# Performance work log

Measured on AMD Instinct MI355X. Metric: run time of the kernel, lower is better.

## Reference

```python
import jax, jax.numpy as jnp
import numpy as np
from jax import lax

NUM_SPLIT = 16
DCT = 7
# top16 frequency indices (first 16 of the top lists)
MAPPER_X = np.array([0, 0, 6, 0, 0, 1, 1, 4, 5, 1, 3, 0, 0, 0, 3, 2], dtype=np.int32)
MAPPER_Y = np.array([0, 1, 0, 5, 2, 0, 2, 0, 0, 6, 0, 4, 6, 3, 5, 2], dtype=np.int32)


def _dct_table():
    pos = np.arange(DCT)
    freq = np.arange(DCT)[:, None]
    d = np.cos(np.pi * freq * (pos + 0.5) / DCT) / np.sqrt(DCT)
    d[1:] *= np.sqrt(2.0)
    return d.astype(np.float32)  # (7, 7): [freq, pos]


def _gconv(x, w, b, groups):
    y = lax.conv_general_dilated(x, w, (2, 2), 'VALID',
                                 dimension_numbers=('NCHW', 'OIHW', 'NCHW'),
                                 feature_group_count=groups)
    return y + b[None, :, None, None]


def setup_inputs() -> dict:
    key = jax.random.key(0)
    ks = jax.random.split(key, 7)
    n, c, h, w = 32, 512, 56, 56
    r = 16
    return {
        'x': jax.random.normal(ks[0], (n, c, h, w), jnp.float32),
        'conv1_w': jax.random.normal(ks[1], (NUM_SPLIT, c // NUM_SPLIT, 3, 3), jnp.float32) * 0.05,
        'conv1_b': jax.random.normal(ks[2], (NUM_SPLIT,), jnp.float32) * 0.05,
        'conv2_w': jax.random.normal(ks[3], (NUM_SPLIT, 1, 3, 3), jnp.float32) * 0.3,
        'conv2_b': jax.random.normal(ks[4], (NUM_SPLIT,), jnp.float32) * 0.3,
        'w1': jax.random.normal(ks[5], (c // r, c), jnp.float32) * 0.05,
        'w2': jax.random.normal(ks[6], (c, c // r), jnp.float32) * 0.2,
    }


def reference(x, conv1_w, conv1_b, conv2_w, conv2_b, w1, w2):
    n, c, h, w = x.shape
    c_part = c // NUM_SPLIT
    D = jnp.asarray(_dct_table(), x.dtype)
    mx = jnp.asarray(MAPPER_X)
    my = jnp.asarray(MAPPER_Y)

    # adaptive_avg_pool2d to 7x7 (h,w divisible by 7 -> exact block mean)
    xp = x.reshape(n, c, DCT, h // DCT, DCT, w // DCT).mean(axis=(3, 5))

    # filters_predicted: grouped conv 7x7 -> 3x3 -> 1x1
    a1 = jax.nn.hard_sigmoid(_gconv(xp, conv1_w, conv1_b, NUM_SPLIT))
    v = _gconv(a1, conv2_w, conv2_b, NUM_SPLIT).reshape(n, NUM_SPLIT)
    # adaptive_avg_pool1d(1 -> 16) repeats v; matmul with ones(16,1) sums -> v * 16
    pred = jnp.clip(v * NUM_SPLIT, 0.0, NUM_SPLIT - 1.1)

    left = pred.astype(jnp.int32)   # (n, 16)
    frac = pred - left
    right = left + 1

    def dct_weights(idx):  # idx (n,16) -> per-split 7x7 DCT filters (n,16,7,7)
        fx = D[mx[idx]]  # (n,16,7)
        fy = D[my[idx]]
        return fx[..., :, None] * fy[..., None, :]

    xp_s = xp.reshape(n, NUM_SPLIT, c_part, DCT, DCT)
    res_l = jnp.einsum('nskhw,nshw->nsk', xp_s, dct_weights(left)) * (1.0 - frac)[:, :, None]
    res_r = jnp.einsum('nskhw,nshw->nsk', xp_s, dct_weights(right)) * frac[:, :, None]
    s = (res_l + res_r).reshape(n, c)

    hmid = jax.nn.hard_sigmoid(s @ w1.T)
    cw = jax.nn.sigmoid(hmid @ w2.T)  # (n, c)
    return x * cw[:, :, None, None]
```

## Files before the change

kernel.cpp:

```cpp
#include <hip/hip_runtime.h>

#define N_   32
#define C_   512
#define H_   56
#define W_   56
#define S_   16
#define CP_  32
#define HW_  (H_*W_)
#define TOT_ ((size_t)N_*C_*HW_)

typedef float f32x4 __attribute__((ext_vector_type(4)));

__constant__ int d_mx[16] = {0,0,6,0,0,1,1,4,5,1,3,0,0,0,3,2};
__constant__ int d_my[16] = {0,1,0,5,2,0,2,0,0,6,0,4,6,3,5,2};

__global__ void __launch_bounds__(256) pool_kernel(const float* __restrict__ x,
                                                   float* __restrict__ xp) {
    __shared__ float part[784];
    int plane = blockIdx.x;
    int t = threadIdx.x;
    const f32x4* src = reinterpret_cast<const f32x4*>(x + (size_t)plane * HW_);
    f32x4 u0 = src[t];
    f32x4 u1 = src[t + 256];
    f32x4 u2 = src[t + 512];
    f32x4 u3;
    if (t < 16) u3 = src[t + 768];
    part[t]       = u0.x + u0.y + u0.z + u0.w;
    part[t + 256] = u1.x + u1.y + u1.z + u1.w;
    part[t + 512] = u2.x + u2.y + u2.z + u2.w;
    if (t < 16) part[t + 768] = u3.x + u3.y + u3.z + u3.w;
    __syncthreads();
    if (t < 49) {
        int rb = t / 7, cb = t - rb * 7;
        const float* p = &part[rb * 8 * 14 + cb * 2];
        float s = 0.f;
#pragma unroll
        for (int r = 0; r < 8; ++r) s += p[r * 14] + p[r * 14 + 1];
        xp[(size_t)plane * 49 + t] = s * (1.0f / 64.0f);
    }
}

__global__ void __launch_bounds__(256) head_kernel(
        const float* __restrict__ xp,
        const float* __restrict__ c1w, const float* __restrict__ c1b,
        const float* __restrict__ c2w, const float* __restrict__ c2b,
        const float* __restrict__ w1,  const float* __restrict__ w2,
        float* __restrict__ cwout) {
    __shared__ float sD[49];
    __shared__ float a1[S_ * 9];
    __shared__ float wcomb[S_ * 49];
    __shared__ float svec[C_];
    __shared__ float hpart[256];
    __shared__ float hmid[32];
    __shared__ float sfrac[S_];
    __shared__ int   sleft[S_];

    const int n = blockIdx.x, t = threadIdx.x;
    const float* xpn = xp + (size_t)n * C_ * 49;

    if (t >= 192 && t < 241) {
        int u = t - 192, f = u / 7, p = u - f * 7;
        float v = cosf(3.14159265358979323846f * f * (p + 0.5f) / 7.0f) * 0.3779644730092272f;
        if (f >= 1) v *= 1.4142135623730951f;
        sD[u] = v;
    }
    if (t < S_ * 9) {
        int s = t / 9, o = t - s * 9, oi = o / 3, oj = o - oi * 3;
        float acc = c1b[s];
        const float* xb = xpn + s * CP_ * 49;
        const float* wb = c1w + s * CP_ * 9;
        for (int ic = 0; ic < CP_; ++ic) {
#pragma unroll
            for (int ki = 0; ki < 3; ++ki)
#pragma unroll
                for (int kj = 0; kj < 3; ++kj)
                    acc += xb[ic * 49 + (oi * 2 + ki) * 7 + (oj * 2 + kj)]
                         * wb[ic * 9 + ki * 3 + kj];
        }
        a1[t] = fminf(fmaxf(acc + 3.f, 0.f), 6.f) * (1.f / 6.f);
    }
    __syncthreads();

    if (t < S_) {
        float acc = c2b[t];
#pragma unroll
        for (int k = 0; k < 9; ++k) acc += a1[t * 9 + k] * c2w[t * 9 + k];
        float pred = fminf(fmaxf(acc * 16.f, 0.f), 14.9f);
        int l = (int)pred;
        sleft[t] = l;
        sfrac[t] = pred - (float)l;
    }
    __syncthreads();

    for (int i = t; i < S_ * 49; i += 256) {
        int s = i / 49, p = i - s * 49, hh = p / 7, ww = p - hh * 7;
        int l = sleft[s], r = l + 1;
        float fr = sfrac[s];
        wcomb[i] = (1.f - fr) * sD[d_mx[l] * 7 + hh] * sD[d_my[l] * 7 + ww]
                 +        fr  * sD[d_mx[r] * 7 + hh] * sD[d_my[r] * 7 + ww];
    }
    __syncthreads();

#pragma unroll
    for (int q = 0; q < 2; ++q) {
        int ch = t + q * 256;
        const float* xb = xpn + ch * 49;
        const float* wb = &wcomb[(ch >> 5) * 49];
        float acc = 0.f;
#pragma unroll
        for (int p = 0; p < 49; ++p) acc += xb[p] * wb[p];
        svec[ch] = acc;
    }
    __syncthreads();

    {
        int o = t >> 3, g = t & 7;
        const f32x4* wv = reinterpret_cast<const f32x4*>(w1 + o * C_ + g * 64);
        const f32x4* sv = reinterpret_cast<const f32x4*>(&svec[g * 64]);
        float acc = 0.f;
#pragma unroll
        for (int j = 0; j < 16; ++j) {
            f32x4 a = sv[j], b = wv[j];
            acc += a.x * b.x + a.y * b.y + a.z * b.z + a.w * b.w;
        }
        hpart[t] = acc;
    }
    __syncthreads();
    if (t < 32) {
        float acc = 0.f;
#pragma unroll
        for (int g = 0; g < 8; ++g) acc += hpart[t * 8 + g];
        hmid[t] = fminf(fmaxf(acc + 3.f, 0.f), 6.f) * (1.f / 6.f);
    }
    __syncthreads();

#pragma unroll
    for (int q = 0; q < 2; ++q) {
        int ch = t + q * 256;
        const f32x4* wr = reinterpret_cast<const f32x4*>(w2 + ch * 32);
        const f32x4* hv = reinterpret_cast<const f32x4*>(hmid);
        float acc = 0.f;
#pragma unroll
        for (int j = 0; j < 8; ++j) {
            f32x4 h = hv[j], b = wr[j];
            acc += h.x * b.x + h.y * b.y + h.z * b.z + h.w * b.w;
        }
        cwout[n * C_ + ch] = 1.f / (1.f + expf(-acc));
    }
}

__global__ void __launch_bounds__(256) scale_kernel(const float* __restrict__ x,
                                                    const float* __restrict__ cw,
                                                    float* __restrict__ out) {
    int plane = blockIdx.x;
    int t = threadIdx.x;
    float wsc = cw[plane];
    const f32x4* src = reinterpret_cast<const f32x4*>(x + (size_t)plane * HW_);
    f32x4* dst = reinterpret_cast<f32x4*>(out + (size_t)plane * HW_);

    f32x4 u0 = src[t];
    f32x4 u1 = src[t + 256];
    f32x4 u2 = src[t + 512];
    f32x4 u3;
    if (t < 16) u3 = src[t + 768];

    u0 *= wsc;
    u1 *= wsc;
    u2 *= wsc;

    __builtin_nontemporal_store(u0, dst + t);
    __builtin_nontemporal_store(u1, dst + t + 256);
    __builtin_nontemporal_store(u2, dst + t + 512);
    if (t < 16) {
        u3 *= wsc;
        __builtin_nontemporal_store(u3, dst + t + 768);
    }
}

extern "C" void kernel_launch(void* const* d_in, const int* in_sizes, int n_in,
                              void* d_out, int out_size, void* d_ws, size_t ws_size,
                              hipStream_t stream) {
    const float* x   = (const float*)d_in[0];
    const float* c1w = (const float*)d_in[1];
    const float* c1b = (const float*)d_in[2];
    const float* c2w = (const float*)d_in[3];
    const float* c2b = (const float*)d_in[4];
    const float* w1  = (const float*)d_in[5];
    const float* w2  = (const float*)d_in[6];
    float* out = (float*)d_out;

    float* xp    = (float*)d_ws;
    float* cwbuf = xp + (size_t)N_ * C_ * 49;

    pool_kernel<<<N_ * C_, 256, 0, stream>>>(x, xp);
    head_kernel<<<N_, 256, 0, stream>>>(xp, c1w, c1b, c2w, c2b, w1, w2, cwbuf);
    scale_kernel<<<N_ * C_, 256, 0, stream>>>(x, cwbuf, out);
}
```

Before: 393.2 us.

## Fuse pooling and head into one kernel using last-block atomic counter

The pooling and head kernels are merged into one kernel. Each block pools one plane, then bumps a per-sample atomic counter, and the last block to finish for a sample runs the head computation. This removes a kernel launch and the serial head kernel that ran only 32 blocks, so head work for each sample can overlap with pooling of other samples. In exchange it adds a memset launch, threadfences and atomics, and the fused kernel uses more shared memory, which may lower occupancy during the bandwidth-bound pooling phase.

After: 1.064 ms. 2.71x slower.

```diff
diff --git a/kernel.cpp b/kernel.cpp
--- a/kernel.cpp
+++ b/kernel.cpp
@@ -14,38 +14,16 @@
 __constant__ int d_mx[16] = {0,0,6,0,0,1,1,4,5,1,3,0,0,0,3,2};
 __constant__ int d_my[16] = {0,1,0,5,2,0,2,0,0,6,0,4,6,3,5,2};
 
-__global__ void __launch_bounds__(256) pool_kernel(const float* __restrict__ x,
-                                                   float* __restrict__ xp) {
-    __shared__ float part[784];
-    int plane = blockIdx.x;
-    int t = threadIdx.x;
-    const f32x4* src = reinterpret_cast<const f32x4*>(x + (size_t)plane * HW_);
-    f32x4 u0 = src[t];
-    f32x4 u1 = src[t + 256];
-    f32x4 u2 = src[t + 512];
-    f32x4 u3;
-    if (t < 16) u3 = src[t + 768];
-    part[t]       = u0.x + u0.y + u0.z + u0.w;
-    part[t + 256] = u1.x + u1.y + u1.z + u1.w;
-    part[t + 512] = u2.x + u2.y + u2.z + u2.w;
-    if (t < 16) part[t + 768] = u3.x + u3.y + u3.z + u3.w;
-    __syncthreads();
-    if (t < 49) {
-        int rb = t / 7, cb = t - rb * 7;
-        const float* p = &part[rb * 8 * 14 + cb * 2];
-        float s = 0.f;
-#pragma unroll
-        for (int r = 0; r < 8; ++r) s += p[r * 14] + p[r * 14 + 1];
-        xp[(size_t)plane * 49 + t] = s * (1.0f / 64.0f);
-    }
-}
-
-__global__ void __launch_bounds__(256) head_kernel(
-        const float* __restrict__ xp,
+__global__ void __launch_bounds__(256) pool_head_kernel(
+        const float* __restrict__ x,
+        float* __restrict__ xp,
+        int* __restrict__ counters,
         const float* __restrict__ c1w, const float* __restrict__ c1b,
         const float* __restrict__ c2w, const float* __restrict__ c2b,
         const float* __restrict__ w1,  const float* __restrict__ w2,
         float* __restrict__ cwout) {
+    __shared__ float part[784];
+    __shared__ int   lastflag;
     __shared__ float sD[49];
     __shared__ float a1[S_ * 9];
     __shared__ float wcomb[S_ * 49];
@@ -55,7 +33,42 @@
     __shared__ float sfrac[S_];
     __shared__ int   sleft[S_];
 
-    const int n = blockIdx.x, t = threadIdx.x;
+    const int plane = blockIdx.x;
+    const int t = threadIdx.x;
+
+    {
+        const f32x4* src = reinterpret_cast<const f32x4*>(x + (size_t)plane * HW_);
+        f32x4 u0 = src[t];
+        f32x4 u1 = src[t + 256];
+        f32x4 u2 = src[t + 512];
+        f32x4 u3;
+        if (t < 16) u3 = src[t + 768];
+        part[t]       = u0.x + u0.y + u0.z + u0.w;
+        part[t + 256] = u1.x + u1.y + u1.z + u1.w;
+        part[t + 512] = u2.x + u2.y + u2.z + u2.w;
+        if (t < 16) part[t + 768] = u3.x + u3.y + u3.z + u3.w;
+        __syncthreads();
+        if (t < 49) {
+            int rb = t / 7, cb = t - rb * 7;
+            const float* p = &part[rb * 8 * 14 + cb * 2];
+            float s = 0.f;
+#pragma unroll
+            for (int r = 0; r < 8; ++r) s += p[r * 14] + p[r * 14 + 1];
+            xp[(size_t)plane * 49 + t] = s * (1.0f / 64.0f);
+        }
+    }
+    __syncthreads();
+
+    if (t == 0) {
+        __threadfence();
+        int old = atomicAdd(&counters[plane >> 9], 1);
+        lastflag = (old == C_ - 1);
+    }
+    __syncthreads();
+    if (!lastflag) return;
+    __threadfence();
+
+    const int n = plane >> 9;
     const float* xpn = xp + (size_t)n * C_ * 49;
 
     if (t >= 192 && t < 241) {
@@ -191,8 +204,10 @@
 
     float* xp    = (float*)d_ws;
     float* cwbuf = xp + (size_t)N_ * C_ * 49;
-
-    pool_kernel<<<N_ * C_, 256, 0, stream>>>(x, xp);
-    head_kernel<<<N_, 256, 0, stream>>>(xp, c1w, c1b, c2w, c2b, w1, w2, cwbuf);
+    int*   cnt   = (int*)(cwbuf + (size_t)N_ * C_);
+
+    hipMemsetAsync(cnt, 0, N_ * sizeof(int), stream);
+    pool_head_kernel<<<N_ * C_, 256, 0, stream>>>(x, xp, cnt, c1w, c1b, c2w, c2b,
+                                                  w1, w2, cwbuf);
     scale_kernel<<<N_ * C_, 256, 0, stream>>>(x, cwbuf, out);
 }
```
